# Performance work log

Measured on AMD Instinct MI355X. Metric: run time of the kernel, lower is better.

## Reference

```python
import jax, jax.numpy as jnp
import numpy as np

B, S, DIM = 1, 2048, 2048
NH, NKV, HD = 32, 8, 64
NREP = NH // NKV
SCALE = 1.0 / float(np.sqrt(HD))
NEG = -1e30


def _apply_rope(q, k, rope_cache):
    # q: (B,S,NH,HD), k: (B,S,NKV,HD); rope_cache: (S, HD) = [cos | sin], each HD//2 wide
    cos = rope_cache[:, : HD // 2][None, :, None, :]  # (1,S,1,HD/2)
    sin = rope_cache[:, HD // 2 :][None, :, None, :]

    def rot(x):
        x1, x2 = x[..., : HD // 2], x[..., HD // 2 :]
        return jnp.concatenate([x1 * cos - x2 * sin, x1 * sin + x2 * cos], axis=-1)

    return rot(q), rot(k)


def setup_inputs() -> dict:
    key = jax.random.key(0)
    ks = jax.random.split(key, 12)
    std = 0.02
    x = jax.random.normal(ks[0], (B, S, DIM), jnp.float32)
    # real rotary cos/sin cache
    inv_freq = 1.0 / (10000.0 ** (np.arange(0, HD, 2, dtype=np.float64) / HD))
    freqs = np.outer(np.arange(S, dtype=np.float64), inv_freq)
    rope_cache = jnp.asarray(
        np.concatenate([np.cos(freqs), np.sin(freqs)], axis=-1), jnp.float32
    )  # (S, HD)
    return {
        "x": x,
        "rope_cache": rope_cache,
        "wq_w": jax.random.normal(ks[1], (NH * HD, DIM), jnp.float32) * std,
        "wq_b": jax.random.normal(ks[2], (NH * HD,), jnp.float32) * std,
        "wk_w": jax.random.normal(ks[3], (NKV * HD, DIM), jnp.float32) * std,
        "wk_b": jax.random.normal(ks[4], (NKV * HD,), jnp.float32) * std,
        "wv_w": jax.random.normal(ks[5], (NKV * HD, DIM), jnp.float32) * std,
        "wv_b": jax.random.normal(ks[6], (NKV * HD,), jnp.float32) * std,
        "wo_w": jax.random.normal(ks[7], (DIM, NH * HD), jnp.float32) * std,
        "wo_b": jax.random.normal(ks[8], (DIM,), jnp.float32) * std,
        "sinks": jax.random.normal(ks[9], (NH,), jnp.float32) * std,
    }


def reference(x, rope_cache, wq_w, wq_b, wk_w, wk_b, wv_w, wv_b, wo_w, wo_b, sinks):
    q = (x @ wq_w.T + wq_b).reshape(B, S, NH, HD)
    k = (x @ wk_w.T + wk_b).reshape(B, S, NKV, HD)
    v = (x @ wv_w.T + wv_b).reshape(B, S, NKV, HD)
    q, k = _apply_rope(q, k, rope_cache)
    q = q.transpose(0, 2, 1, 3)  # (B,NH,S,HD)
    k = jnp.repeat(k.transpose(0, 2, 1, 3), NREP, axis=1)  # GQA expand -> (B,NH,S,HD)
    v = jnp.repeat(v.transpose(0, 2, 1, 3), NREP, axis=1)
    scores = jnp.einsum("bhqd,bhkd->bhqk", q, k) * SCALE
    causal = jnp.tril(jnp.ones((S, S), bool))
    scores = jnp.where(causal[None, None], scores, NEG)
    lse = jax.scipy.special.logsumexp(scores, axis=-1)  # (B,NH,S)
    attn = jnp.exp(scores - lse[..., None])
    out = jnp.einsum("bhqk,bhkd->bhqd", attn, v)
    sink_scale = jax.nn.sigmoid(lse - sinks[None, :, None])  # (B,NH,S)
    out = out * sink_scale[..., None]
    out = out.transpose(0, 2, 1, 3).reshape(B, S, NH * HD)
    return out @ wo_w.T + wo_b
```

## Files before the change

### kernel.cpp

```cpp
#include <hip/hip_runtime.h>

typedef unsigned short ushort_t;
typedef short s8v __attribute__((ext_vector_type(8)));
typedef float f4v __attribute__((ext_vector_type(4)));

#define DIMK   2048
#define NHEAD  32
#define HDIM   64
#define SCALE_LOG2E 0.18033688f

__device__ __forceinline__ unsigned short f2bf(float f) {
    unsigned u = __float_as_uint(f);
    u += 0x7fffu + ((u >> 16) & 1u);
    return (unsigned short)(u >> 16);
}

__device__ __forceinline__ unsigned pack_bf2(float f0, float f1) {
    unsigned a = __float_as_uint(f0) + 0x8000u;
    unsigned b = __float_as_uint(f1) + 0x8000u;
    return __builtin_amdgcn_perm(b, a, 0x07060302u);
}

__device__ __forceinline__ float fexp2(float x) {
#if __has_builtin(__builtin_amdgcn_exp2f)
    return __builtin_amdgcn_exp2f(x);
#else
    return exp2f(x);
#endif
}

__device__ __forceinline__ void gll16(const void* g, void* l) {
    __builtin_amdgcn_global_load_lds(
        (const __attribute__((address_space(1))) void*)g,
        (__attribute__((address_space(3))) void*)l, 16, 0, 0);
}

__device__ __forceinline__ f4v mfma16(s8v a, s8v b, f4v c) {
    return __builtin_amdgcn_mfma_f32_16x16x32_bf16(a, b, c, 0, 0, 0);
}

__global__ __launch_bounds__(256) void cast_all(
    const float* __restrict__ x,  const float* __restrict__ wq,
    const float* __restrict__ wk, const float* __restrict__ wv,
    const float* __restrict__ wo,
    ushort_t* __restrict__ xb,  ushort_t* __restrict__ wqb,
    ushort_t* __restrict__ wkb, ushort_t* __restrict__ wvb,
    ushort_t* __restrict__ wob)
{
    int i = blockIdx.x * 256 + threadIdx.x;
    const float* src; ushort_t* dst;
    if      (i < 1048576) { src = x;  dst = xb; }
    else if (i < 2097152) { src = wq; dst = wqb; i -= 1048576; }
    else if (i < 2359296) { src = wk; dst = wkb; i -= 2097152; }
    else if (i < 2621440) { src = wv; dst = wvb; i -= 2359296; }
    else                  { src = wo; dst = wob; i -= 2621440; }
    float4 v = ((const float4*)src)[i];
    ushort4 o;
    o.x = f2bf(v.x); o.y = f2bf(v.y); o.z = f2bf(v.z); o.w = f2bf(v.w);
    ((ushort4*)dst)[i] = o;
}

__device__ __forceinline__ void gemm_core64(
    const ushort_t* __restrict__ A, const ushort_t* __restrict__ Bt,
    int bm, int bn64, ushort_t* As, ushort_t* Bs, f4v acc[2][4])
{
    const int tid  = threadIdx.x;
    const int wave = tid >> 6, lane = tid & 63;
    const int c = lane & 15, q4 = lane >> 4;

    const ushort_t* ag = A  + (size_t)(bm * 128 + wave * 32 + (lane >> 2)) * DIMK + (lane & 3) * 8;
    const ushort_t* bg = Bt + (size_t)(bn64 * 64 + wave * 16 + (lane >> 2)) * DIMK + (lane & 3) * 8;
    ushort_t* as0 = As + (wave * 32) * 32;
    ushort_t* as1 = As + (wave * 32 + 16) * 32;
    ushort_t* bs0 = Bs + (wave * 16) * 32;

    for (int k0 = 0; k0 < DIMK; k0 += 32) {
        gll16(ag + k0,             as0);
        gll16(ag + 16 * DIMK + k0, as1);
        gll16(bg + k0,             bs0);
        __syncthreads();
        s8v af[2], bfv[4];
#pragma unroll
        for (int mt = 0; mt < 2; ++mt)
            af[mt] = *(const s8v*)(As + (wave * 32 + mt * 16 + c) * 32 + q4 * 8);
#pragma unroll
        for (int nt = 0; nt < 4; ++nt)
            bfv[nt] = *(const s8v*)(Bs + (nt * 16 + c) * 32 + q4 * 8);
#pragma unroll
        for (int mt = 0; mt < 2; ++mt)
#pragma unroll
            for (int nt = 0; nt < 4; ++nt)
                acc[mt][nt] = mfma16(af[mt], bfv[nt], acc[mt][nt]);
        __syncthreads();
    }
}

__global__ __launch_bounds__(256) void qkv_gemm(
    const ushort_t* __restrict__ Xb,
    const ushort_t* __restrict__ Wqb, const ushort_t* __restrict__ Wkb, const ushort_t* __restrict__ Wvb,
    const float* __restrict__ biasq, const float* __restrict__ biask, const float* __restrict__ biasv,
    const float* __restrict__ rope,
    ushort_t* __restrict__ Qo, ushort_t* __restrict__ Kblk, ushort_t* __restrict__ Vblk)
{
    __shared__ ushort_t As[128 * 32], Bs[64 * 32];
    const int nb = blockIdx.x, bm = blockIdx.y;
    const ushort_t* Bt; const float* bias; int nbl, mode;
    if      (nb < 32) { Bt = Wqb; bias = biasq; nbl = nb;      mode = 0; }
    else if (nb < 40) { Bt = Wkb; bias = biask; nbl = nb - 32; mode = 1; }
    else              { Bt = Wvb; bias = biasv; nbl = nb - 40; mode = 2; }

    const f4v fz = {0.f, 0.f, 0.f, 0.f};
    f4v acc[2][4];
    for (int i = 0; i < 2; ++i) for (int j = 0; j < 4; ++j) acc[i][j] = fz;

    gemm_core64(Xb, Bt, bm, nbl, As, Bs, acc);

    const int tid = threadIdx.x, wave = tid >> 6, lane = tid & 63;
    const int c = lane & 15, q4 = lane >> 4;

    if (mode == 0) {
#pragma unroll
        for (int mt = 0; mt < 2; ++mt)
#pragma unroll
            for (int r = 0; r < 4; ++r) {
                int row = bm * 128 + wave * 32 + mt * 16 + q4 * 4 + r;
                const float* rp = rope + row * 64;
#pragma unroll
                for (int nt = 0; nt < 2; ++nt) {
                    int d   = nt * 16 + c;
                    int col = nbl * 64 + d;
                    float cs = rp[d], sn = rp[32 + d];
                    float x1 = acc[mt][nt][r]     + bias[col];
                    float x2 = acc[mt][nt + 2][r] + bias[col + 32];
                    Qo[(size_t)row * 2048 + col]      = f2bf((x1 * cs - x2 * sn) * SCALE_LOG2E);
                    Qo[(size_t)row * 2048 + col + 32] = f2bf((x1 * sn + x2 * cs) * SCALE_LOG2E);
                }
            }
    } else if (mode == 1) {
#pragma unroll
        for (int mt = 0; mt < 2; ++mt)
#pragma unroll
            for (int r = 0; r < 4; ++r) {
                int row = bm * 128 + wave * 32 + mt * 16 + q4 * 4 + r;
                const float* rp = rope + row * 64;
                int kt = row >> 6, ntk = (row & 63) >> 4, ck = row & 15;
#pragma unroll
                for (int nt = 0; nt < 2; ++nt) {
                    int d   = nt * 16 + c;
                    int col = nbl * 64 + d;
                    float cs = rp[d], sn = rp[32 + d];
                    float x1 = acc[mt][nt][r]     + bias[col];
                    float x2 = acc[mt][nt + 2][r] + bias[col + 32];
                    float o1 = x1 * cs - x2 * sn;
                    float o2 = x1 * sn + x2 * cs;
                    {   int dd = d;       int kc = dd >> 5, q4k = (dd >> 3) & 3, j = dd & 7;
                        Kblk[(((((size_t)nbl * 32 + kt) * 2 + kc) * 4 + ntk) * 64 + q4k * 16 + ck) * 8 + j] = f2bf(o1); }
                    {   int dd = d + 32;  int kc = dd >> 5, q4k = (dd >> 3) & 3, j = dd & 7;
                        Kblk[(((((size_t)nbl * 32 + kt) * 2 + kc) * 4 + ntk) * 64 + q4k * 16 + ck) * 8 + j] = f2bf(o2); }
                }
            }
    } else {
#pragma unroll
        for (int mt = 0; mt < 2; ++mt)
#pragma unroll
            for (int nt = 0; nt < 4; ++nt)
#pragma unroll
                for (int r = 0; r < 4; ++r) {
                    int row = bm * 128 + wave * 32 + mt * 16 + q4 * 4 + r;
                    int col = nbl * 64 + nt * 16 + c;
                    int kt = row >> 6, K64 = row & 63;
                    int kp = (K64 & 15) * 4 + (K64 >> 4);
                    int kc = kp >> 5, q4v = (kp >> 3) & 3, j = kp & 7;
                    Vblk[(((((size_t)nbl * 32 + kt) * 2 + kc) * 4 + nt) * 64 + q4v * 16 + c) * 8 + j]
                        = f2bf(acc[mt][nt][r] + bias[col]);
                }
    }
}

__global__ __launch_bounds__(256) void proj_gemm(
    const ushort_t* __restrict__ Ob, const ushort_t* __restrict__ Wob,
    const float* __restrict__ bias, float* __restrict__ Co)
{
    __shared__ ushort_t As[128 * 32], Bs[64 * 32];
    const f4v fz = {0.f, 0.f, 0.f, 0.f};
    f4v acc[2][4];
    for (int i = 0; i < 2; ++i) for (int j = 0; j < 4; ++j) acc[i][j] = fz;

    gemm_core64(Ob, Wob, blockIdx.y, blockIdx.x, As, Bs, acc);

    const int tid = threadIdx.x, wave = tid >> 6, lane = tid & 63;
    const int c = lane & 15, q4 = lane >> 4;
#pragma unroll
    for (int mt = 0; mt < 2; ++mt)
#pragma unroll
        for (int nt = 0; nt < 4; ++nt)
#pragma unroll
            for (int r = 0; r < 4; ++r) {
                int row = blockIdx.y * 128 + wave * 32 + mt * 16 + q4 * 4 + r;
                int col = blockIdx.x * 64 + nt * 16 + c;
                Co[(size_t)row * 2048 + col] = acc[mt][nt][r] + bias[col];
            }
}

__global__ __launch_bounds__(256) void attn_kernel(
    const ushort_t* __restrict__ Qb,
    const ushort_t* __restrict__ Kblk,
    const ushort_t* __restrict__ Vblk,
    const float* __restrict__ sinks,
    ushort_t* __restrict__ Ob)
{
    __shared__ ushort_t Ps[4][16 * 72];
    const int t = 31 - blockIdx.x, h = blockIdx.y, kvh = h >> 2;
    const int tid = threadIdx.x, wave = tid >> 6, lane = tid & 63;
    const int c = lane & 15, q4 = lane >> 4;
    const int q0 = t * 64 + wave * 16;
    ushort_t* Pw = &Ps[wave][0];

    s8v qf[2];
#pragma unroll
    for (int kc = 0; kc < 2; ++kc)
        qf[kc] = *(const s8v*)(Qb + (size_t)(q0 + c) * 2048 + h * 64 + kc * 32 + q4 * 8);

    const f4v fz = {0.f, 0.f, 0.f, 0.f};
    f4v Oacc[4];
    float Lp[4];
#pragma unroll
    for (int dt = 0; dt < 4; ++dt) Oacc[dt] = fz;
#pragma unroll
    for (int r = 0; r < 4; ++r) Lp[r] = 0.f;

    const ushort_t* kbase = Kblk + (size_t)kvh * 32 * 4096;
    const ushort_t* vbase = Vblk + (size_t)kvh * 32 * 4096;

    for (int kt = 0; kt <= t; ++kt) {
        const ushort_t* kp = kbase + (size_t)kt * 4096;
        const ushort_t* vp = vbase + (size_t)kt * 4096;
        s8v kf[4][2], vf[4][2];
#pragma unroll
        for (int kc = 0; kc < 2; ++kc)
#pragma unroll
            for (int nt = 0; nt < 4; ++nt) {
                kf[nt][kc] = *(const s8v*)(kp + ((kc * 4 + nt) * 64 + lane) * 8);
                vf[nt][kc] = *(const s8v*)(vp + ((kc * 4 + nt) * 64 + lane) * 8);
            }

        f4v S[4];
#pragma unroll
        for (int nt = 0; nt < 4; ++nt) S[nt] = fz;
#pragma unroll
        for (int kc = 0; kc < 2; ++kc)
#pragma unroll
            for (int nt = 0; nt < 4; ++nt)
                S[nt] = mfma16(qf[kc], kf[nt][kc], S[nt]);

        if (kt == t) {
#pragma unroll
            for (int nt = 0; nt < 4; ++nt) {
                int key = t * 64 + nt * 16 + c;
#pragma unroll
                for (int r = 0; r < 4; ++r) {
                    int qrow = q0 + q4 * 4 + r;
                    if (key > qrow) S[nt][r] = -1.0e30f;
                }
            }
        }

#pragma unroll
        for (int r = 0; r < 4; ++r) {
            float p0 = fexp2(S[0][r]), p1 = fexp2(S[1][r]);
            float p2 = fexp2(S[2][r]), p3 = fexp2(S[3][r]);
            Lp[r] += (p0 + p1) + (p2 + p3);
            int2 w_; w_.x = (int)pack_bf2(p0, p1); w_.y = (int)pack_bf2(p2, p3);
            *(int2*)(Pw + (q4 * 4 + r) * 72 + c * 4) = w_;
        }
        s8v pa[2];
#pragma unroll
        for (int kc = 0; kc < 2; ++kc)
            pa[kc] = *(const s8v*)(Pw + c * 72 + kc * 32 + q4 * 8);
#pragma unroll
        for (int kc = 0; kc < 2; ++kc)
#pragma unroll
            for (int dt = 0; dt < 4; ++dt)
                Oacc[dt] = mfma16(pa[kc], vf[dt][kc], Oacc[dt]);
    }

#pragma unroll
    for (int r = 0; r < 4; ++r)
#pragma unroll
        for (int off = 1; off < 16; off <<= 1)
            Lp[r] += __shfl_xor(Lp[r], off);

    const float sk = sinks[h];
#pragma unroll
    for (int r = 0; r < 4; ++r) {
        float L = Lp[r];
        float lse = __logf(L);
        float sig = 1.f / (1.f + __expf(sk - lse));
        float sc  = sig / L;
        int row = q0 + q4 * 4 + r;
#pragma unroll
        for (int dt = 0; dt < 4; ++dt)
            Ob[(size_t)row * 2048 + h * 64 + dt * 16 + c] = f2bf(Oacc[dt][r] * sc);
    }
}

extern "C" void kernel_launch(void* const* d_in, const int* in_sizes, int n_in,
                              void* d_out, int out_size, void* d_ws, size_t ws_size,
                              hipStream_t stream)
{
    (void)in_sizes; (void)n_in; (void)out_size; (void)ws_size;
    const float* x     = (const float*)d_in[0];
    const float* rope  = (const float*)d_in[1];
    const float* wq    = (const float*)d_in[2];
    const float* qb    = (const float*)d_in[3];
    const float* wk    = (const float*)d_in[4];
    const float* kb    = (const float*)d_in[5];
    const float* wv    = (const float*)d_in[6];
    const float* vb    = (const float*)d_in[7];
    const float* wo    = (const float*)d_in[8];
    const float* wob_f = (const float*)d_in[9];
    const float* sinks = (const float*)d_in[10];
    float* out = (float*)d_out;

    char* ws = (char*)d_ws;
    ushort_t* xb   = (ushort_t*)(ws);
    ushort_t* wqb  = (ushort_t*)(ws + (8ull  << 20));
    ushort_t* wkb  = (ushort_t*)(ws + (16ull << 20));
    ushort_t* wvb  = (ushort_t*)(ws + (18ull << 20));
    ushort_t* wob  = (ushort_t*)(ws + (20ull << 20));
    ushort_t* qo   = (ushort_t*)(ws + (28ull << 20));
    ushort_t* kblk = (ushort_t*)(ws + (36ull << 20));
    ushort_t* vblk = (ushort_t*)(ws + (38ull << 20));
    ushort_t* ao   = (ushort_t*)(ws + (40ull << 20));

    cast_all<<<14336, 256, 0, stream>>>(x, wq, wk, wv, wo, xb, wqb, wkb, wvb, wob);
    qkv_gemm<<<dim3(48, 16), 256, 0, stream>>>(xb, wqb, wkb, wvb, qb, kb, vb, rope, qo, kblk, vblk);
    attn_kernel<<<dim3(32, 32), 256, 0, stream>>>(qo, kblk, vblk, sinks, ao);
    proj_gemm<<<dim3(32, 16), 256, 0, stream>>>(ao, wob, wob_f, out);
}
```

Before: 265.0 us.

## Stage QKV epilogue through LDS and pair causal tiles with 32-row waves in attention

The QKV GEMM epilogue now writes rotated Q, K and V into shared memory and then stores them to global with coalesced 16-byte writes instead of scattered 2-byte stores. The attention kernel gives each wave 32 query rows (two MFMA row tiles), so every K/V fragment loaded from global is reused twice. Each block pairs a short causal tile with a long one (p and 31-p), which balances work and halves the grid. In exchange the kernel uses more registers and LDS per wave, and a block now finishes only when its long-tile waves do.

```diff
diff --git a/kernel.cpp b/kernel.cpp
--- a/kernel.cpp
+++ b/kernel.cpp
@@ -102,7 +102,9 @@
     const float* __restrict__ rope,
     ushort_t* __restrict__ Qo, ushort_t* __restrict__ Kblk, ushort_t* __restrict__ Vblk)
 {
-    __shared__ ushort_t As[128 * 32], Bs[64 * 32];
+    __shared__ ushort_t SM[8192];
+    ushort_t* As = SM;
+    ushort_t* Bs = SM + 4096;
     const int nb = blockIdx.x, bm = blockIdx.y;
     const ushort_t* Bt; const float* bias; int nbl, mode;
     if      (nb < 32) { Bt = Wqb; bias = biasq; nbl = nb;      mode = 0; }
@@ -123,7 +125,8 @@
         for (int mt = 0; mt < 2; ++mt)
 #pragma unroll
             for (int r = 0; r < 4; ++r) {
-                int row = bm * 128 + wave * 32 + mt * 16 + q4 * 4 + r;
+                int rowl = wave * 32 + mt * 16 + q4 * 4 + r;
+                int row  = bm * 128 + rowl;
                 const float* rp = rope + row * 64;
 #pragma unroll
                 for (int nt = 0; nt < 2; ++nt) {
@@ -132,8 +135,8 @@
                     float cs = rp[d], sn = rp[32 + d];
                     float x1 = acc[mt][nt][r]     + bias[col];
                     float x2 = acc[mt][nt + 2][r] + bias[col + 32];
-                    Qo[(size_t)row * 2048 + col]      = f2bf((x1 * cs - x2 * sn) * SCALE_LOG2E);
-                    Qo[(size_t)row * 2048 + col + 32] = f2bf((x1 * sn + x2 * cs) * SCALE_LOG2E);
+                    SM[rowl * 64 + d]      = f2bf((x1 * cs - x2 * sn) * SCALE_LOG2E);
+                    SM[rowl * 64 + d + 32] = f2bf((x1 * sn + x2 * cs) * SCALE_LOG2E);
                 }
             }
     } else if (mode == 1) {
@@ -141,9 +144,11 @@
         for (int mt = 0; mt < 2; ++mt)
 #pragma unroll
             for (int r = 0; r < 4; ++r) {
-                int row = bm * 128 + wave * 32 + mt * 16 + q4 * 4 + r;
+                int rowl = wave * 32 + mt * 16 + q4 * 4 + r;
+                int row  = bm * 128 + rowl;
                 const float* rp = rope + row * 64;
-                int kt = row >> 6, ntk = (row & 63) >> 4, ck = row & 15;
+                int tl  = rowl >> 6;
+                int ntk = (rowl & 63) >> 4, ck = rowl & 15;
 #pragma unroll
                 for (int nt = 0; nt < 2; ++nt) {
                     int d   = nt * 16 + c;
@@ -154,9 +159,9 @@
                     float o1 = x1 * cs - x2 * sn;
                     float o2 = x1 * sn + x2 * cs;
                     {   int dd = d;       int kc = dd >> 5, q4k = (dd >> 3) & 3, j = dd & 7;
-                        Kblk[(((((size_t)nbl * 32 + kt) * 2 + kc) * 4 + ntk) * 64 + q4k * 16 + ck) * 8 + j] = f2bf(o1); }
+                        SM[tl * 4096 + ((kc * 4 + ntk) * 64 + q4k * 16 + ck) * 8 + j] = f2bf(o1); }
                     {   int dd = d + 32;  int kc = dd >> 5, q4k = (dd >> 3) & 3, j = dd & 7;
-                        Kblk[(((((size_t)nbl * 32 + kt) * 2 + kc) * 4 + ntk) * 64 + q4k * 16 + ck) * 8 + j] = f2bf(o2); }
+                        SM[tl * 4096 + ((kc * 4 + ntk) * 64 + q4k * 16 + ck) * 8 + j] = f2bf(o2); }
                 }
             }
     } else {
@@ -166,14 +171,32 @@
             for (int nt = 0; nt < 4; ++nt)
 #pragma unroll
                 for (int r = 0; r < 4; ++r) {
-                    int row = bm * 128 + wave * 32 + mt * 16 + q4 * 4 + r;
-                    int col = nbl * 64 + nt * 16 + c;
-                    int kt = row >> 6, K64 = row & 63;
+                    int rowl = wave * 32 + mt * 16 + q4 * 4 + r;
+                    int col  = nbl * 64 + nt * 16 + c;
+                    int tl = rowl >> 6, K64 = rowl & 63;
                     int kp = (K64 & 15) * 4 + (K64 >> 4);
                     int kc = kp >> 5, q4v = (kp >> 3) & 3, j = kp & 7;
-                    Vblk[(((((size_t)nbl * 32 + kt) * 2 + kc) * 4 + nt) * 64 + q4v * 16 + c) * 8 + j]
+                    SM[tl * 4096 + ((kc * 4 + nt) * 64 + q4v * 16 + c) * 8 + j]
                         = f2bf(acc[mt][nt][r] + bias[col]);
                 }
+    }
+    __syncthreads();
+
+    if (mode == 0) {
+#pragma unroll
+        for (int i = 0; i < 4; ++i) {
+            int idx  = i * 256 + tid;
+            int rowl = idx >> 3, c8 = (idx & 7) * 8;
+            *(int4*)(Qo + (size_t)(bm * 128 + rowl) * 2048 + nbl * 64 + c8)
+                = *(const int4*)(SM + idx * 8);
+        }
+    } else {
+        ushort_t* dstb = (mode == 1 ? Kblk : Vblk) + ((size_t)nbl * 32 + bm * 2) * 4096;
+#pragma unroll
+        for (int i = 0; i < 4; ++i) {
+            int idx = i * 256 + tid;
+            *(int4*)(dstb + idx * 8) = *(const int4*)(SM + idx * 8);
+        }
     }
 }
 
@@ -181,7 +204,9 @@
     const ushort_t* __restrict__ Ob, const ushort_t* __restrict__ Wob,
     const float* __restrict__ bias, float* __restrict__ Co)
 {
-    __shared__ ushort_t As[128 * 32], Bs[64 * 32];
+    __shared__ ushort_t SM[8192];
+    ushort_t* As = SM;
+    ushort_t* Bs = SM + 4096;
     const f4v fz = {0.f, 0.f, 0.f, 0.f};
     f4v acc[2][4];
     for (int i = 0; i < 2; ++i) for (int j = 0; j < 4; ++j) acc[i][j] = fz;
@@ -209,25 +234,31 @@
     const float* __restrict__ sinks,
     ushort_t* __restrict__ Ob)
 {
-    __shared__ ushort_t Ps[4][16 * 72];
-    const int t = 31 - blockIdx.x, h = blockIdx.y, kvh = h >> 2;
+    __shared__ ushort_t Ps[4][32 * 72];
+    const int p = blockIdx.x, h = blockIdx.y, kvh = h >> 2;
     const int tid = threadIdx.x, wave = tid >> 6, lane = tid & 63;
     const int c = lane & 15, q4 = lane >> 4;
-    const int q0 = t * 64 + wave * 16;
+    const int t  = (wave < 2) ? p : (31 - p);
+    const int q0 = t * 64 + (wave & 1) * 32;
     ushort_t* Pw = &Ps[wave][0];
 
-    s8v qf[2];
-#pragma unroll
-    for (int kc = 0; kc < 2; ++kc)
-        qf[kc] = *(const s8v*)(Qb + (size_t)(q0 + c) * 2048 + h * 64 + kc * 32 + q4 * 8);
+    s8v qf[2][2];
+#pragma unroll
+    for (int mi = 0; mi < 2; ++mi)
+#pragma unroll
+        for (int kc = 0; kc < 2; ++kc)
+            qf[mi][kc] = *(const s8v*)(Qb + (size_t)(q0 + mi * 16 + c) * 2048 + h * 64 + kc * 32 + q4 * 8);
 
     const f4v fz = {0.f, 0.f, 0.f, 0.f};
-    f4v Oacc[4];
-    float Lp[4];
-#pragma unroll
-    for (int dt = 0; dt < 4; ++dt) Oacc[dt] = fz;
-#pragma unroll
-    for (int r = 0; r < 4; ++r) Lp[r] = 0.f;
+    f4v Oacc[2][4];
+    float Lp[2][4];
+#pragma unroll
+    for (int mi = 0; mi < 2; ++mi) {
+#pragma unroll
+        for (int dt = 0; dt < 4; ++dt) Oacc[mi][dt] = fz;
+#pragma unroll
+        for (int r = 0; r < 4; ++r) Lp[mi][r] = 0.f;
+    }
 
     const ushort_t* kbase = Kblk + (size_t)kvh * 32 * 4096;
     const ushort_t* vbase = Vblk + (size_t)kvh * 32 * 4096;
@@ -244,64 +275,80 @@
                 vf[nt][kc] = *(const s8v*)(vp + ((kc * 4 + nt) * 64 + lane) * 8);
             }
 
-        f4v S[4];
-#pragma unroll
-        for (int nt = 0; nt < 4; ++nt) S[nt] = fz;
+        f4v S[2][4];
+#pragma unroll
+        for (int mi = 0; mi < 2; ++mi)
+#pragma unroll
+            for (int nt = 0; nt < 4; ++nt) S[mi][nt] = fz;
 #pragma unroll
         for (int kc = 0; kc < 2; ++kc)
 #pragma unroll
             for (int nt = 0; nt < 4; ++nt)
-                S[nt] = mfma16(qf[kc], kf[nt][kc], S[nt]);
+#pragma unroll
+                for (int mi = 0; mi < 2; ++mi)
+                    S[mi][nt] = mfma16(qf[mi][kc], kf[nt][kc], S[mi][nt]);
 
         if (kt == t) {
 #pragma unroll
-            for (int nt = 0; nt < 4; ++nt) {
-                int key = t * 64 + nt * 16 + c;
-#pragma unroll
-                for (int r = 0; r < 4; ++r) {
-                    int qrow = q0 + q4 * 4 + r;
-                    if (key > qrow) S[nt][r] = -1.0e30f;
+            for (int mi = 0; mi < 2; ++mi)
+#pragma unroll
+                for (int nt = 0; nt < 4; ++nt) {
+                    int key = t * 64 + nt * 16 + c;
+#pragma unroll
+                    for (int r = 0; r < 4; ++r) {
+                        int qrow = q0 + mi * 16 + q4 * 4 + r;
+                        if (key > qrow) S[mi][nt][r] = -1.0e30f;
+                    }
                 }
-            }
         }
 
 #pragma unroll
+        for (int mi = 0; mi < 2; ++mi)
+#pragma unroll
+            for (int r = 0; r < 4; ++r) {
+                float p0 = fexp2(S[mi][0][r]), p1 = fexp2(S[mi][1][r]);
+                float p2 = fexp2(S[mi][2][r]), p3 = fexp2(S[mi][3][r]);
+                Lp[mi][r] += (p0 + p1) + (p2 + p3);
+                int2 w_; w_.x = (int)pack_bf2(p0, p1); w_.y = (int)pack_bf2(p2, p3);
+                *(int2*)(Pw + (mi * 16 + q4 * 4 + r) * 72 + c * 4) = w_;
+            }
+        s8v pa[2][2];
+#pragma unroll
+        for (int mi = 0; mi < 2; ++mi)
+#pragma unroll
+            for (int kc = 0; kc < 2; ++kc)
+                pa[mi][kc] = *(const s8v*)(Pw + (mi * 16 + c) * 72 + kc * 32 + q4 * 8);
+#pragma unroll
+        for (int kc = 0; kc < 2; ++kc)
+#pragma unroll
+            for (int dt = 0; dt < 4; ++dt)
+#pragma unroll
+                for (int mi = 0; mi < 2; ++mi)
+                    Oacc[mi][dt] = mfma16(pa[mi][kc], vf[dt][kc], Oacc[mi][dt]);
+    }
+
+#pragma unroll
+    for (int mi = 0; mi < 2; ++mi)
+#pragma unroll
+        for (int r = 0; r < 4; ++r)
+#pragma unroll
+            for (int off = 1; off < 16; off <<= 1)
+                Lp[mi][r] += __shfl_xor(Lp[mi][r], off);
+
+    const float sk = sinks[h];
+#pragma unroll
+    for (int mi = 0; mi < 2; ++mi)
+#pragma unroll
         for (int r = 0; r < 4; ++r) {
-            float p0 = fexp2(S[0][r]), p1 = fexp2(S[1][r]);
-            float p2 = fexp2(S[2][r]), p3 = fexp2(S[3][r]);
-            Lp[r] += (p0 + p1) + (p2 + p3);
-            int2 w_; w_.x = (int)pack_bf2(p0, p1); w_.y = (int)pack_bf2(p2, p3);
-            *(int2*)(Pw + (q4 * 4 + r) * 72 + c * 4) = w_;
+            float L = Lp[mi][r];
+            float lse = __logf(L);
+            float sig = 1.f / (1.f + __expf(sk - lse));
+            float sc  = sig / L;
+            int row = q0 + mi * 16 + q4 * 4 + r;
+#pragma unroll
+            for (int dt = 0; dt < 4; ++dt)
+                Ob[(size_t)row * 2048 + h * 64 + dt * 16 + c] = f2bf(Oacc[mi][dt][r] * sc);
         }
-        s8v pa[2];
-#pragma unroll
-        for (int kc = 0; kc < 2; ++kc)
-            pa[kc] = *(const s8v*)(Pw + c * 72 + kc * 32 + q4 * 8);
-#pragma unroll
-        for (int kc = 0; kc < 2; ++kc)
-#pragma unroll
-            for (int dt = 0; dt < 4; ++dt)
-                Oacc[dt] = mfma16(pa[kc], vf[dt][kc], Oacc[dt]);
-    }
-
-#pragma unroll
-    for (int r = 0; r < 4; ++r)
-#pragma unroll
-        for (int off = 1; off < 16; off <<= 1)
-            Lp[r] += __shfl_xor(Lp[r], off);
-
-    const float sk = sinks[h];
-#pragma unroll
-    for (int r = 0; r < 4; ++r) {
-        float L = Lp[r];
-        float lse = __logf(L);
-        float sig = 1.f / (1.f + __expf(sk - lse));
-        float sc  = sig / L;
-        int row = q0 + q4 * 4 + r;
-#pragma unroll
-        for (int dt = 0; dt < 4; ++dt)
-            Ob[(size_t)row * 2048 + h * 64 + dt * 16 + c] = f2bf(Oacc[dt][r] * sc);
-    }
 }
 
 extern "C" void kernel_launch(void* const* d_in, const int* in_sizes, int n_in,
@@ -335,6 +382,6 @@
 
     cast_all<<<14336, 256, 0, stream>>>(x, wq, wk, wv, wo, xb, wqb, wkb, wvb, wob);
     qkv_gemm<<<dim3(48, 16), 256, 0, stream>>>(xb, wqb, wkb, wvb, qb, kb, vb, rope, qo, kblk, vblk);
-    attn_kernel<<<dim3(32, 32), 256, 0, stream>>>(qo, kblk, vblk, sinks, ao);
+    attn_kernel<<<dim3(16, 32), 256, 0, stream>>>(qo, kblk, vblk, sinks, ao);
     proj_gemm<<<dim3(32, 16), 256, 0, stream>>>(ao, wob, wob_f, out);
 }
```

Result: faster. 239.3 us (-9.7%).
